# Kernel tuning notes

Measured on AMD Instinct MI355X. Metric: run time of the kernel, lower is better.

## Reference

```python
import jax, jax.numpy as jnp
import numpy as np

K = 8  # knn_graph(k=8, loop=True): self-loop kept, so self is among the k nearest


def knn_idx(x, k):
    # x: [N, F]. Pairwise squared distances via the expansion trick.
    x2 = jnp.sum(x * x, axis=-1)                      # [N]
    d = x2[:, None] + x2[None, :] - 2.0 * (x @ x.T)   # [N, N]
    _, idx = jax.lax.top_k(-d, k)                     # [N, k] nearest (incl. self)
    return idx


def edge_conv(x, idx, W1, b1, W2, b2):
    # PyG EdgeConv: message = nn(cat([x_i, x_j - x_i])), aggr='max'.
    # Every node has exactly k incoming edges, so scatter-max == max over the k axis.
    n, f = x.shape
    k = idx.shape[1]
    xi = x[:, None, :]                                # [N, 1, F] center
    xj = x[idx]                                       # [N, k, F] neighbors (gather)
    e = jnp.concatenate([jnp.broadcast_to(xi, (n, k, f)), xj - xi], axis=-1)  # [N,k,2F]
    h = jax.nn.relu(e @ W1 + b1) @ W2 + b2            # [N, k, out]
    return jnp.max(h, axis=1)                         # [N, out]


def setup_inputs() -> dict:
    key = jax.random.key(0)
    ks = jax.random.split(key, 9)
    B, N, F = 2, 4096, 3
    H0, H1, OUT = 64, 128, 256

    def lin(kw, fan_in, fan_out):
        bound = 1.0 / np.sqrt(fan_in)
        kw1, kw2 = jax.random.split(kw)
        W = jax.random.uniform(kw1, (fan_in, fan_out), jnp.float32, -bound, bound)
        b = jax.random.uniform(kw2, (fan_out,), jnp.float32, -bound, bound)
        return W, b

    W1, b1 = lin(ks[0], 2 * F, H0)
    W2, b2 = lin(ks[1], H0, H1)
    W3, b3 = lin(ks[2], 2 * H1, H1)
    W4, b4 = lin(ks[3], H1, OUT)
    point_cloud = jax.random.normal(ks[4], (B, N, F), jnp.float32)
    return {"point_cloud": point_cloud, "W1": W1, "b1": b1, "W2": W2, "b2": b2,
            "W3": W3, "b3": b3, "W4": W4, "b4": b4}


def reference(point_cloud, W1, b1, W2, b2, W3, b3, W4, b4):
    B, N, F = point_cloud.shape
    pts = point_cloud.reshape(B * N, F)               # knn over ALL B*N points (no batch vec)
    idx = knn_idx(jax.lax.stop_gradient(pts), K)      # [B*N, K]
    x = jax.nn.relu(edge_conv(pts, idx, W1, b1, W2, b2))
    x = edge_conv(x, idx, W3, b3, W4, b4)
    return x.reshape(B, N, -1)
```

## Files before the change

### kernel.cpp

```cpp
#include <hip/hip_runtime.h>

#define NPTS 8192
#define NSLICE 64
#define SLICE_LEN (NPTS / NSLICE)
#define KNN 8
#define SURV_CAP 48
#define TQ 32

typedef short bf16x8 __attribute__((ext_vector_type(8)));
typedef float f32x4 __attribute__((ext_vector_type(4)));

__device__ __forceinline__ unsigned short f2bf(float x) {
  unsigned int u = __float_as_uint(x);
  return (unsigned short)((u + 0x7FFF + ((u >> 16) & 1)) >> 16);
}
__device__ __forceinline__ float bf2f(unsigned short s) {
  return __uint_as_float(((unsigned int)s) << 16);
}

__device__ __forceinline__ float dist_exact(float qx, float qy, float qz,
                                            float q2, float px, float py,
                                            float pz, float p2) {
#pragma clang fp contract(off)
  float dot = __fmaf_rn(qz, pz, __fmaf_rn(qy, py, __fmul_rn(qx, px)));
  float t1 = __fadd_rn(q2, p2);
  return __fadd_rn(t1, __fmul_rn(-2.0f, dot));
}

__device__ __forceinline__ float norm2_exact(float x, float y, float z) {
#pragma clang fp contract(off)
  return __fadd_rn(__fadd_rn(__fmul_rn(x, x), __fmul_rn(y, y)),
                   __fmul_rn(z, z));
}

__device__ __forceinline__ float med3(float a, float b, float c) {
  return __builtin_amdgcn_fmed3f(a, b, c);
}

__device__ __forceinline__ double pack_key(float d, int idx) {
  unsigned int ub = __float_as_uint(d);
  ub ^= (((unsigned int)((int)ub >> 31)) | 0x80000000u);
  unsigned int lo = (ub << 13) | (unsigned int)idx;
  unsigned int hi = 0x3ff00000u | (ub >> 19);
  return __hiloint2double((int)hi, (int)lo);
}

#define KEY_DECL                                                            \
  const double KINF = __longlong_as_double(0x7ff0000000000000LL);           \
  double k0 = KINF, k1 = KINF, k2 = KINF, k3 = KINF, k4 = KINF, k5 = KINF,  \
         k6 = KINF, k7 = KINF;
#define KB1(s)                                                              \
  {                                                                         \
    double mn = fmin(carry, k##s);                                          \
    carry = fmax(carry, k##s);                                              \
    k##s = mn;                                                              \
  }
#define KEY_INSERT(key)                                                     \
  {                                                                         \
    double carry = (key);                                                   \
    KB1(0) KB1(1) KB1(2) KB1(3) KB1(4) KB1(5) KB1(6) KB1(7)                 \
  }

#define VINS(dv)                                                            \
  {                                                                         \
    float dd = (dv);                                                        \
    v7 = med3(dd, v6, v7);                                                  \
    v6 = med3(dd, v5, v6);                                                  \
    v5 = med3(dd, v4, v5);                                                  \
    v4 = med3(dd, v3, v4);                                                  \
    v3 = med3(dd, v2, v3);                                                  \
    v2 = med3(dd, v1, v2);                                                  \
    v1 = med3(dd, v0, v1);                                                  \
    v0 = fminf(dd, v0);                                                     \
  }

#define VDECL                                                               \
  const float FINF = __uint_as_float(0x7f800000u);                          \
  float v0 = FINF, v1 = FINF, v2 = FINF, v3 = FINF, v4 = FINF, v5 = FINF,   \
        v6 = FINF, v7 = FINF;

#define VINS2(dv)                                                           \
  {                                                                         \
    float dd = (dv);                                                        \
    s1 = med3(dd, s0, s1);                                                  \
    s0 = fminf(dd, s0);                                                     \
  }

__global__ __launch_bounds__(256) void prep_kernel(
    const float* __restrict__ W4, const float* __restrict__ pts,
    const float* __restrict__ W2, const float* __restrict__ W3,
    unsigned short* __restrict__ W4ht, unsigned short* __restrict__ W4lt,
    unsigned short* __restrict__ W2th, unsigned short* __restrict__ W2tl,
    unsigned short* __restrict__ W3th, unsigned short* __restrict__ W3tl,
    float4* __restrict__ pts4) {
  const int id = blockIdx.x * 256 + threadIdx.x;
  const int k = id >> 8, c = id & 255;
  {
    float v = W4[k * 256 + c];
    unsigned short hi = f2bf(v);
    unsigned short lo = f2bf(v - bf2f(hi));
    W4ht[c * 128 + k] = hi;
    W4lt[c * 128 + k] = lo;
  }
  {
    float v3 = (c < 128) ? W3[k * 128 + c] : W3[(128 + k) * 128 + (c - 128)];
    unsigned short h3 = f2bf(v3);
    W3th[c * 128 + k] = h3;
    W3tl[c * 128 + k] = f2bf(v3 - bf2f(h3));
  }
  if (id < NPTS) {
    float x = pts[id * 3 + 0];
    float y = pts[id * 3 + 1];
    float z = pts[id * 3 + 2];
    pts4[id] = make_float4(x, y, z, norm2_exact(x, y, z));
    const int kk = id >> 7, cc = id & 127;
    float v2 = W2[kk * 128 + cc];
    unsigned short h2 = f2bf(v2);
    W2th[cc * 64 + kk] = h2;
    W2tl[cc * 64 + kk] = f2bf(v2 - bf2f(h2));
  }
}

__global__ __launch_bounds__(256) void knn_vals_kernel(
    const float4* __restrict__ pts4, float* __restrict__ part_v) {
  __shared__ float4 sp[SLICE_LEN];
  const int t = threadIdx.x;
  const int q = blockIdx.x * 256 + t;
  const int jbase = blockIdx.y * SLICE_LEN;
  for (int p = t; p < SLICE_LEN; p += 256) sp[p] = pts4[jbase + p];
  __syncthreads();
  const float4 qp = pts4[q];
  const float qx = qp.x, qy = qp.y, qz = qp.z, q2 = qp.w;
  const float FINF = __uint_as_float(0x7f800000u);
  float s0 = FINF, s1 = FINF;
  for (int p = 0; p < SLICE_LEN; p += 8) {
    float4 c0 = sp[p + 0];
    float4 c1 = sp[p + 1];
    float4 c2 = sp[p + 2];
    float4 c3 = sp[p + 3];
    float4 c4 = sp[p + 4];
    float4 c5 = sp[p + 5];
    float4 c6 = sp[p + 6];
    float4 c7 = sp[p + 7];
    float d0 = dist_exact(qx, qy, qz, q2, c0.x, c0.y, c0.z, c0.w);
    float d1 = dist_exact(qx, qy, qz, q2, c1.x, c1.y, c1.z, c1.w);
    float d2 = dist_exact(qx, qy, qz, q2, c2.x, c2.y, c2.z, c2.w);
    float d3 = dist_exact(qx, qy, qz, q2, c3.x, c3.y, c3.z, c3.w);
    float d4 = dist_exact(qx, qy, qz, q2, c4.x, c4.y, c4.z, c4.w);
    float d5 = dist_exact(qx, qy, qz, q2, c5.x, c5.y, c5.z, c5.w);
    float d6 = dist_exact(qx, qy, qz, q2, c6.x, c6.y, c6.z, c6.w);
    float d7 = dist_exact(qx, qy, qz, q2, c7.x, c7.y, c7.z, c7.w);
    VINS2(d0);
    VINS2(d1);
    VINS2(d2);
    VINS2(d3);
    VINS2(d4);
    VINS2(d5);
    VINS2(d6);
    VINS2(d7);
  }
  float* o = &part_v[(size_t)(blockIdx.y * 2) * NPTS + q];
  o[0 * NPTS] = s0;
  o[1 * NPTS] = s1;
}

__global__ __launch_bounds__(256) void knn_thresh_kernel(
    const float* __restrict__ part_v, float* __restrict__ thr,
    unsigned long long* __restrict__ mask) {
  __shared__ float v8s[TQ][8][9];
  __shared__ float smin[TQ][65];
  const int t = threadIdx.x;
  const int lq = t >> 3, c = t & 7;
  const int q = blockIdx.x * TQ + lq;
  {
    VDECL;
#pragma unroll
    for (int s8 = 0; s8 < 8; ++s8) {
      const int s = c * 8 + s8;
      const float* col = &part_v[(size_t)(s * 2) * NPTS + q];
      float a0 = col[0 * (size_t)NPTS];
      float a1 = col[1 * (size_t)NPTS];
      smin[lq][s] = a0;
      VINS(a0);
      VINS(a1);
    }
    v8s[lq][c][0] = v0;
    v8s[lq][c][1] = v1;
    v8s[lq][c][2] = v2;
    v8s[lq][c][3] = v3;
    v8s[lq][c][4] = v4;
    v8s[lq][c][5] = v5;
    v8s[lq][c][6] = v6;
    v8s[lq][c][7] = v7;
  }
  __syncthreads();
  if (c == 0) {
    VDECL;
#pragma unroll
    for (int s = 0; s < 8; ++s) {
      VINS(v8s[lq][s][0]);
      VINS(v8s[lq][s][1]);
      VINS(v8s[lq][s][2]);
      VINS(v8s[lq][s][3]);
      VINS(v8s[lq][s][4]);
      VINS(v8s[lq][s][5]);
      VINS(v8s[lq][s][6]);
      VINS(v8s[lq][s][7]);
    }
    const float tcol = v7 + fabsf(v7) * 4e-5f + 1e-20f;
    const float tmask = v7 + fabsf(v7) * 8e-5f + 2e-20f;
    unsigned long long mk = 0;
#pragma unroll
    for (int s = 0; s < NSLICE; ++s) {
      if (smin[lq][s] <= tmask) mk |= (1ull << s);
    }
    thr[q] = tcol;
    mask[q] = mk;
  }
}

__global__ __launch_bounds__(256) void knn_collect_kernel(
    const float4* __restrict__ pts4, const float* __restrict__ thr,
    const unsigned long long* __restrict__ mask, int* __restrict__ nbr) {
  __shared__ double keybuf[4][SURV_CAP];
  __shared__ int scnt[4];
  const int t = threadIdx.x;
  const int wv = t >> 6;
  const int lane = t & 63;
  const int q = blockIdx.x * 4 + wv;
  if (lane == 0) scnt[wv] = 0;
  __syncthreads();
  const float4 qp = pts4[q];
  const float qx = qp.x, qy = qp.y, qz = qp.z, q2 = qp.w;
  const float thrq = thr[q];
  unsigned long long m = mask[q];
  while (m) {
    const int s = (int)__ffsll(m) - 1;
    m &= m - 1;
    const int base = s * SLICE_LEN;
#pragma unroll
    for (int r = 0; r < SLICE_LEN / 64; ++r) {
      const int j = base + r * 64 + lane;
      const float4 cp = pts4[j];
      const float d = dist_exact(qx, qy, qz, q2, cp.x, cp.y, cp.z, cp.w);
      if (d <= thrq) {
        int slot = atomicAdd(&scnt[wv], 1);
        if (slot < SURV_CAP) keybuf[wv][slot] = pack_key(d, j);
      }
    }
  }
  __syncthreads();
  if (lane == 0) {
    int c = scnt[wv];
    if (c > SURV_CAP) c = SURV_CAP;
    KEY_DECL;
    for (int u = 0; u < c; ++u) {
      KEY_INSERT(keybuf[wv][u]);
    }
    int* o = &nbr[q * KNN];
    o[0] = __double2loint(k0) & 0x1fff;
    o[1] = __double2loint(k1) & 0x1fff;
    o[2] = __double2loint(k2) & 0x1fff;
    o[3] = __double2loint(k3) & 0x1fff;
    o[4] = __double2loint(k4) & 0x1fff;
    o[5] = __double2loint(k5) & 0x1fff;
    o[6] = __double2loint(k6) & 0x1fff;
    o[7] = __double2loint(k7) & 0x1fff;
  }
}

__global__ __launch_bounds__(256) void gemm1_fused_kernel(
    const float* __restrict__ pts, const int* __restrict__ nbr,
    const float* __restrict__ W1, const float* __restrict__ b1,
    const unsigned short* __restrict__ W2th,
    const unsigned short* __restrict__ W2tl, const float* __restrict__ b2,
    float* __restrict__ y) {
  __shared__ float es[64][6];
  __shared__ float W1s[6][64];
  __shared__ float b1s[64];
  __shared__ unsigned short H1h[64 * 72];
  __shared__ unsigned short H1l[64 * 72];
  __shared__ unsigned short Wth[64 * 72];
  __shared__ unsigned short Wtl[64 * 72];
  const int t = threadIdx.x;
  const int rowBase = blockIdx.y * 64;
  const int colBase = blockIdx.x * 64;

  for (int idx = t; idx < 384; idx += 256) W1s[idx >> 6][idx & 63] = W1[idx];
  if (t < 64) b1s[t] = b1[t];
  {
    const int colloc = t >> 2, kq = (t & 3) * 16;
    const size_t src = (size_t)(colBase + colloc) * 64 + kq;
    *(uint4*)&Wth[colloc * 72 + kq] = *(const uint4*)&W2th[src];
    *(uint4*)&Wth[colloc * 72 + kq + 8] = *(const uint4*)&W2th[src + 8];
    *(uint4*)&Wtl[colloc * 72 + kq] = *(const uint4*)&W2tl[src];
    *(uint4*)&Wtl[colloc * 72 + kq + 8] = *(const uint4*)&W2tl[src + 8];
  }
  if (t < 64) {
    int e = rowBase + t;
    int i = e >> 3;
    int j = nbr[e];
    float xi0 = pts[i * 3], xi1 = pts[i * 3 + 1], xi2 = pts[i * 3 + 2];
    es[t][0] = xi0;
    es[t][1] = xi1;
    es[t][2] = xi2;
    es[t][3] = pts[j * 3] - xi0;
    es[t][4] = pts[j * 3 + 1] - xi1;
    es[t][5] = pts[j * 3 + 2] - xi2;
  }
  __syncthreads();

  {
    const int e = t & 63, k0 = (t >> 6) * 16;
    const float f0 = es[e][0], f1 = es[e][1], f2 = es[e][2];
    const float f3 = es[e][3], f4 = es[e][4], f5 = es[e][5];
    float h[16];
#pragma unroll
    for (int k = 0; k < 16; ++k) {
      int c = k0 + k;
      float v = b1s[c];
      v = fmaf(f0, W1s[0][c], v);
      v = fmaf(f1, W1s[1][c], v);
      v = fmaf(f2, W1s[2][c], v);
      v = fmaf(f3, W1s[3][c], v);
      v = fmaf(f4, W1s[4][c], v);
      v = fmaf(f5, W1s[5][c], v);
      h[k] = fmaxf(v, 0.0f);
    }
    unsigned int hp[8], lp[8];
#pragma unroll
    for (int u = 0; u < 8; ++u) {
      unsigned short h0 = f2bf(h[2 * u]), h1 = f2bf(h[2 * u + 1]);
      hp[u] = (unsigned int)h0 | ((unsigned int)h1 << 16);
      unsigned short l0 = f2bf(h[2 * u] - bf2f(h0));
      unsigned short l1 = f2bf(h[2 * u + 1] - bf2f(h1));
      lp[u] = (unsigned int)l0 | ((unsigned int)l1 << 16);
    }
    *(uint4*)&H1h[e * 72 + k0] = make_uint4(hp[0], hp[1], hp[2], hp[3]);
    *(uint4*)&H1h[e * 72 + k0 + 8] = make_uint4(hp[4], hp[5], hp[6], hp[7]);
    *(uint4*)&H1l[e * 72 + k0] = make_uint4(lp[0], lp[1], lp[2], lp[3]);
    *(uint4*)&H1l[e * 72 + k0 + 8] = make_uint4(lp[4], lp[5], lp[6], lp[7]);
  }
  __syncthreads();

  const int lane = t & 63, w = t >> 6;
  const int qq = lane >> 4, nidx = lane & 15;
  f32x4 acc[4];
#pragma unroll
  for (int nt = 0; nt < 4; ++nt) acc[nt] = (f32x4){0.f, 0.f, 0.f, 0.f};
  bf16x8 ah0, ah1, al0, al1;
  {
    const int row = w * 16 + nidx;
    ah0 = *(const bf16x8*)&H1h[row * 72 + qq * 8];
    ah1 = *(const bf16x8*)&H1h[row * 72 + 32 + qq * 8];
    al0 = *(const bf16x8*)&H1l[row * 72 + qq * 8];
    al1 = *(const bf16x8*)&H1l[row * 72 + 32 + qq * 8];
  }
#pragma unroll
  for (int nt = 0; nt < 4; ++nt) {
    const int col = nt * 16 + nidx;
    bf16x8 bh0 = *(const bf16x8*)&Wth[col * 72 + qq * 8];
    bf16x8 bh1 = *(const bf16x8*)&Wth[col * 72 + 32 + qq * 8];
    bf16x8 bl0 = *(const bf16x8*)&Wtl[col * 72 + qq * 8];
    bf16x8 bl1 = *(const bf16x8*)&Wtl[col * 72 + 32 + qq * 8];
    acc[nt] = __builtin_amdgcn_mfma_f32_16x16x32_bf16(ah0, bh0, acc[nt], 0, 0, 0);
    acc[nt] = __builtin_amdgcn_mfma_f32_16x16x32_bf16(ah1, bh1, acc[nt], 0, 0, 0);
    acc[nt] = __builtin_amdgcn_mfma_f32_16x16x32_bf16(ah0, bl0, acc[nt], 0, 0, 0);
    acc[nt] = __builtin_amdgcn_mfma_f32_16x16x32_bf16(ah1, bl1, acc[nt], 0, 0, 0);
    acc[nt] = __builtin_amdgcn_mfma_f32_16x16x32_bf16(al0, bh0, acc[nt], 0, 0, 0);
    acc[nt] = __builtin_amdgcn_mfma_f32_16x16x32_bf16(al1, bh1, acc[nt], 0, 0, 0);
  }

  const int pt = blockIdx.y * 8 + 2 * w + (qq >> 1);
#pragma unroll
  for (int nt = 0; nt < 4; ++nt) {
    f32x4 a = acc[nt];
    float m = fmaxf(fmaxf(a[0], a[1]), fmaxf(a[2], a[3]));
    float o = fmaxf(m, __shfl_xor(m, 16, 64));
    if ((qq & 1) == 0) {
      int cg = colBase + nt * 16 + nidx;
      y[(size_t)pt * 128 + cg] = fmaxf(o + b2[cg], 0.0f);
    }
  }
}

__global__ __launch_bounds__(256) void gemm_ac_mfma_kernel(
    const float* __restrict__ y, const unsigned short* __restrict__ W3th,
    const unsigned short* __restrict__ W3tl, const float* __restrict__ bias,
    float* __restrict__ AC) {
  __shared__ unsigned short Ah[128 * 40];
  __shared__ unsigned short Al[128 * 40];
  __shared__ unsigned short Bh[128 * 40];
  __shared__ unsigned short Bl[128 * 40];
  const int t = threadIdx.x;
  const int rowBase = blockIdx.y * 128;
  const int colBase = blockIdx.x * 128;
  const int eloc = t >> 1, hh = t & 1;
  const int kb = hh * 16;
  const int lane = t & 63, w = t >> 6;
  const int q = lane >> 4, nidx = lane & 15;

  f32x4 acc[2][8];
#pragma unroll
  for (int mt = 0; mt < 2; ++mt)
#pragma unroll
    for (int nt = 0; nt < 8; ++nt) acc[mt][nt] = (f32x4){0.f, 0.f, 0.f, 0.f};

  for (int p = 0; p < 4; ++p) {
    const int k0 = p * 32;
    {
      const float* src = &y[(size_t)(rowBase + eloc) * 128 + k0 + kb];
      float h[16];
      *(float4*)&h[0] = *(const float4*)&src[0];
      *(float4*)&h[4] = *(const float4*)&src[4];
      *(float4*)&h[8] = *(const float4*)&src[8];
      *(float4*)&h[12] = *(const float4*)&src[12];
      unsigned int hp[8], lp[8];
#pragma unroll
      for (int u = 0; u < 8; ++u) {
        unsigned short h0 = f2bf(h[2 * u]), h1 = f2bf(h[2 * u + 1]);
        hp[u] = (unsigned int)h0 | ((unsigned int)h1 << 16);
        unsigned short l0 = f2bf(h[2 * u] - bf2f(h0));
        unsigned short l1 = f2bf(h[2 * u + 1] - bf2f(h1));
        lp[u] = (unsigned int)l0 | ((unsigned int)l1 << 16);
      }
      *(uint4*)&Ah[eloc * 40 + kb] = make_uint4(hp[0], hp[1], hp[2], hp[3]);
      *(uint4*)&Ah[eloc * 40 + kb + 8] = make_uint4(hp[4], hp[5], hp[6], hp[7]);
      *(uint4*)&Al[eloc * 40 + kb] = make_uint4(lp[0], lp[1], lp[2], lp[3]);
      *(uint4*)&Al[eloc * 40 + kb + 8] = make_uint4(lp[4], lp[5], lp[6], lp[7]);
    }
    {
      const size_t src = (size_t)(colBase + eloc) * 128 + k0 + kb;
      *(uint4*)&Bh[eloc * 40 + kb] = *(const uint4*)&W3th[src];
      *(uint4*)&Bh[eloc * 40 + kb + 8] = *(const uint4*)&W3th[src + 8];
      *(uint4*)&Bl[eloc * 40 + kb] = *(const uint4*)&W3tl[src];
      *(uint4*)&Bl[eloc * 40 + kb + 8] = *(const uint4*)&W3tl[src + 8];
    }
    __syncthreads();
    bf16x8 ah[2], al[2];
#pragma unroll
    for (int mt = 0; mt < 2; ++mt) {
      int row = w * 32 + mt * 16 + nidx;
      ah[mt] = *(const bf16x8*)&Ah[row * 40 + q * 8];
      al[mt] = *(const bf16x8*)&Al[row * 40 + q * 8];
    }
#pragma unroll
    for (int nt = 0; nt < 8; ++nt) {
      int col = nt * 16 + nidx;
      bf16x8 bh = *(const bf16x8*)&Bh[col * 40 + q * 8];
      bf16x8 bl = *(const bf16x8*)&Bl[col * 40 + q * 8];
#pragma unroll
      for (int mt = 0; mt < 2; ++mt) {
        acc[mt][nt] = __builtin_amdgcn_mfma_f32_16x16x32_bf16(
            ah[mt], bh, acc[mt][nt], 0, 0, 0);
        acc[mt][nt] = __builtin_amdgcn_mfma_f32_16x16x32_bf16(
            ah[mt], bl, acc[mt][nt], 0, 0, 0);
        acc[mt][nt] = __builtin_amdgcn_mfma_f32_16x16x32_bf16(
            al[mt], bh, acc[mt][nt], 0, 0, 0);
      }
    }
    __syncthreads();
  }

#pragma unroll
  for (int mt = 0; mt < 2; ++mt) {
    const int rowb = rowBase + w * 32 + mt * 16 + q * 4;
#pragma unroll
    for (int nt = 0; nt < 8; ++nt) {
      f32x4 a = acc[mt][nt];
      const int cg = colBase + nt * 16 + nidx;
      const float bb = (cg < 128) ? bias[cg] : 0.0f;
#pragma unroll
      for (int reg = 0; reg < 4; ++reg) {
        AC[(size_t)(rowb + reg) * 256 + cg] = a[reg] + bb;
      }
    }
  }
}

__global__ __launch_bounds__(256) void gemm2_mfma_kernel(
    const float* __restrict__ AC, const int* __restrict__ nbr,
    const unsigned short* __restrict__ W4ht,
    const unsigned short* __restrict__ W4lt, const float* __restrict__ b4,
    float* __restrict__ out) {
  __shared__ unsigned short H2h[128 * 40];
  __shared__ unsigned short H2l[128 * 40];
  __shared__ unsigned short Wth[128 * 40];
  __shared__ unsigned short Wtl[128 * 40];
  const int t = threadIdx.x;
  const int rowBase = blockIdx.y * 128;
  const int colBase = blockIdx.x * 128;
  const int eloc = t >> 1, hh = t & 1;
  const int kb = hh * 16;
  const int edge = rowBase + eloc;
  const int ip = edge >> 3;
  const int jp = nbr[edge];
  const float* ai_p = AC + (size_t)ip * 256;
  const float* ci_p = ai_p + 128;
  const float* cj_p = AC + (size_t)jp * 256 + 128;
  const int lane = t & 63;
  const int w = t >> 6;
  const int q = lane >> 4;
  const int nidx = lane & 15;

  f32x4 acc[2][8];
#pragma unroll
  for (int mt = 0; mt < 2; ++mt)
#pragma unroll
    for (int nt = 0; nt < 8; ++nt) acc[mt][nt] = (f32x4){0.f, 0.f, 0.f, 0.f};

  for (int p = 0; p < 4; ++p) {
    const int k0 = p * 32;
    {
      float h2[16];
      const float4* a4 = (const float4*)(ai_p + k0 + kb);
      const float4* c4 = (const float4*)(ci_p + k0 + kb);
      const float4* d4 = (const float4*)(cj_p + k0 + kb);
#pragma unroll
      for (int u = 0; u < 4; ++u) {
        float4 a = a4[u], c = c4[u], d = d4[u];
        h2[u * 4 + 0] = fmaxf(a.x + d.x - c.x, 0.f);
        h2[u * 4 + 1] = fmaxf(a.y + d.y - c.y, 0.f);
        h2[u * 4 + 2] = fmaxf(a.z + d.z - c.z, 0.f);
        h2[u * 4 + 3] = fmaxf(a.w + d.w - c.w, 0.f);
      }
      unsigned int hp[8], lp[8];
#pragma unroll
      for (int u = 0; u < 8; ++u) {
        unsigned short h0 = f2bf(h2[2 * u]), h1 = f2bf(h2[2 * u + 1]);
        hp[u] = (unsigned int)h0 | ((unsigned int)h1 << 16);
        unsigned short l0 = f2bf(h2[2 * u] - bf2f(h0));
        unsigned short l1 = f2bf(h2[2 * u + 1] - bf2f(h1));
        lp[u] = (unsigned int)l0 | ((unsigned int)l1 << 16);
      }
      *(uint4*)&H2h[eloc * 40 + kb] = make_uint4(hp[0], hp[1], hp[2], hp[3]);
      *(uint4*)&H2h[eloc * 40 + kb + 8] =
          make_uint4(hp[4], hp[5], hp[6], hp[7]);
      *(uint4*)&H2l[eloc * 40 + kb] = make_uint4(lp[0], lp[1], lp[2], lp[3]);
      *(uint4*)&H2l[eloc * 40 + kb + 8] =
          make_uint4(lp[4], lp[5], lp[6], lp[7]);
    }
    {
      const size_t src = (size_t)(colBase + eloc) * 128 + k0 + kb;
      *(uint4*)&Wth[eloc * 40 + kb] = *(const uint4*)&W4ht[src];
      *(uint4*)&Wth[eloc * 40 + kb + 8] = *(const uint4*)&W4ht[src + 8];
      *(uint4*)&Wtl[eloc * 40 + kb] = *(const uint4*)&W4lt[src];
      *(uint4*)&Wtl[eloc * 40 + kb + 8] = *(const uint4*)&W4lt[src + 8];
    }
    __syncthreads();
    bf16x8 ah[2], al[2];
#pragma unroll
    for (int mt = 0; mt < 2; ++mt) {
      int row = w * 32 + mt * 16 + nidx;
      ah[mt] = *(const bf16x8*)&H2h[row * 40 + q * 8];
      al[mt] = *(const bf16x8*)&H2l[row * 40 + q * 8];
    }
#pragma unroll
    for (int nt = 0; nt < 8; ++nt) {
      int col = nt * 16 + nidx;
      bf16x8 bh = *(const bf16x8*)&Wth[col * 40 + q * 8];
      bf16x8 bl = *(const bf16x8*)&Wtl[col * 40 + q * 8];
#pragma unroll
      for (int mt = 0; mt < 2; ++mt) {
        acc[mt][nt] = __builtin_amdgcn_mfma_f32_16x16x32_bf16(
            ah[mt], bh, acc[mt][nt], 0, 0, 0);
        acc[mt][nt] = __builtin_amdgcn_mfma_f32_16x16x32_bf16(
            ah[mt], bl, acc[mt][nt], 0, 0, 0);
        acc[mt][nt] = __builtin_amdgcn_mfma_f32_16x16x32_bf16(
            al[mt], bh, acc[mt][nt], 0, 0, 0);
      }
    }
    __syncthreads();
  }

#pragma unroll
  for (int mt = 0; mt < 2; ++mt) {
    const int ebase = rowBase + w * 32 + mt * 16;
    const int pt0 = ebase >> 3;
#pragma unroll
    for (int nt = 0; nt < 8; ++nt) {
      f32x4 a = acc[mt][nt];
      float m = fmaxf(fmaxf(a[0], a[1]), fmaxf(a[2], a[3]));
      float o = fmaxf(m, __shfl_xor(m, 16, 64));
      int cg = colBase + nt * 16 + nidx;
      if (q == 0) {
        out[(size_t)pt0 * 256 + cg] = o + b4[cg];
      } else if (q == 2) {
        out[(size_t)(pt0 + 1) * 256 + cg] = o + b4[cg];
      }
    }
  }
}

extern "C" void kernel_launch(void* const* d_in, const int* in_sizes, int n_in,
                              void* d_out, int out_size, void* d_ws,
                              size_t ws_size, hipStream_t stream) {
  const float* pts = (const float*)d_in[0];
  const float* W1 = (const float*)d_in[1];
  const float* b1 = (const float*)d_in[2];
  const float* W2 = (const float*)d_in[3];
  const float* b2 = (const float*)d_in[4];
  const float* W3 = (const float*)d_in[5];
  const float* b3 = (const float*)d_in[6];
  const float* W4 = (const float*)d_in[7];
  const float* b4 = (const float*)d_in[8];
  float* out = (float*)d_out;

  float* w = (float*)d_ws;
  float* part_v = w;
  float* thr = w + 4194304;
  int* nbr = (int*)(w + 4202496);
  float* y = w + 4268032;
  unsigned long long* mask = (unsigned long long*)(w + 5316608);
  unsigned short* W4ht = (unsigned short*)(w + 5332992);
  unsigned short* W4lt = (unsigned short*)(w + 5349376);
  float4* pts4 = (float4*)(w + 5365760);
  unsigned short* W2th = (unsigned short*)(w + 5398528);
  unsigned short* W2tl = (unsigned short*)(w + 5402624);
  unsigned short* W3th = (unsigned short*)(w + 5406720);
  unsigned short* W3tl = (unsigned short*)(w + 5423104);
  float* AC = w;

  prep_kernel<<<128, 256, 0, stream>>>(W4, pts, W2, W3, W4ht, W4lt, W2th,
                                       W2tl, W3th, W3tl, pts4);

  knn_vals_kernel<<<dim3(32, NSLICE), 256, 0, stream>>>(pts4, part_v);
  knn_thresh_kernel<<<NPTS / TQ, 256, 0, stream>>>(part_v, thr, mask);
  knn_collect_kernel<<<2048, 256, 0, stream>>>(pts4, thr, mask, nbr);

  gemm1_fused_kernel<<<dim3(2, 1024), 256, 0, stream>>>(pts, nbr, W1, b1,
                                                        W2th, W2tl, b2, y);

  gemm_ac_mfma_kernel<<<dim3(2, 64), 256, 0, stream>>>(y, W3th, W3tl, b3, AC);
  gemm2_mfma_kernel<<<dim3(2, 512), 256, 0, stream>>>(AC, nbr, W4ht, W4lt, b4,
                                                      out);
}
```

Before: 156.4 us.

## Fold prep kernel into knn kernels and widen GEMM tiles to full columns

Removes the separate prep launch. The float4 point packing now happens inside knn_vals, and the bf16 hi/lo weight splitting happens in the first 128 blocks of knn_collect. gemm1 and gemm2 now compute all output columns per block instead of splitting columns across two blocks, which avoids re-gathering neighbor rows and recomputing the first MLP layer twice. The costs are more accumulator registers and larger LDS weight tiles, which may reduce occupancy, plus a halved grid size.

```diff
diff --git a/kernel.cpp b/kernel.cpp
--- a/kernel.cpp
+++ b/kernel.cpp
@@ -86,51 +86,24 @@
     s0 = fminf(dd, s0);                                                     \
   }
 
-__global__ __launch_bounds__(256) void prep_kernel(
-    const float* __restrict__ W4, const float* __restrict__ pts,
-    const float* __restrict__ W2, const float* __restrict__ W3,
-    unsigned short* __restrict__ W4ht, unsigned short* __restrict__ W4lt,
-    unsigned short* __restrict__ W2th, unsigned short* __restrict__ W2tl,
-    unsigned short* __restrict__ W3th, unsigned short* __restrict__ W3tl,
+__global__ __launch_bounds__(256) void knn_vals_kernel(
+    const float* __restrict__ pts, float* __restrict__ part_v,
     float4* __restrict__ pts4) {
-  const int id = blockIdx.x * 256 + threadIdx.x;
-  const int k = id >> 8, c = id & 255;
-  {
-    float v = W4[k * 256 + c];
-    unsigned short hi = f2bf(v);
-    unsigned short lo = f2bf(v - bf2f(hi));
-    W4ht[c * 128 + k] = hi;
-    W4lt[c * 128 + k] = lo;
-  }
-  {
-    float v3 = (c < 128) ? W3[k * 128 + c] : W3[(128 + k) * 128 + (c - 128)];
-    unsigned short h3 = f2bf(v3);
-    W3th[c * 128 + k] = h3;
-    W3tl[c * 128 + k] = f2bf(v3 - bf2f(h3));
-  }
-  if (id < NPTS) {
-    float x = pts[id * 3 + 0];
-    float y = pts[id * 3 + 1];
-    float z = pts[id * 3 + 2];
-    pts4[id] = make_float4(x, y, z, norm2_exact(x, y, z));
-    const int kk = id >> 7, cc = id & 127;
-    float v2 = W2[kk * 128 + cc];
-    unsigned short h2 = f2bf(v2);
-    W2th[cc * 64 + kk] = h2;
-    W2tl[cc * 64 + kk] = f2bf(v2 - bf2f(h2));
-  }
-}
-
-__global__ __launch_bounds__(256) void knn_vals_kernel(
-    const float4* __restrict__ pts4, float* __restrict__ part_v) {
   __shared__ float4 sp[SLICE_LEN];
   const int t = threadIdx.x;
   const int q = blockIdx.x * 256 + t;
   const int jbase = blockIdx.y * SLICE_LEN;
-  for (int p = t; p < SLICE_LEN; p += 256) sp[p] = pts4[jbase + p];
+  for (int p = t; p < SLICE_LEN; p += 256) {
+    float x = pts[(jbase + p) * 3 + 0];
+    float yy = pts[(jbase + p) * 3 + 1];
+    float z = pts[(jbase + p) * 3 + 2];
+    float4 v = make_float4(x, yy, z, norm2_exact(x, yy, z));
+    sp[p] = v;
+    if (blockIdx.x == 0) pts4[jbase + p] = v;
+  }
   __syncthreads();
-  const float4 qp = pts4[q];
-  const float qx = qp.x, qy = qp.y, qz = qp.z, q2 = qp.w;
+  const float qx = pts[q * 3 + 0], qy = pts[q * 3 + 1], qz = pts[q * 3 + 2];
+  const float q2 = norm2_exact(qx, qy, qz);
   const float FINF = __uint_as_float(0x7f800000u);
   float s0 = FINF, s1 = FINF;
   for (int p = 0; p < SLICE_LEN; p += 8) {
@@ -221,10 +194,38 @@
 
 __global__ __launch_bounds__(256) void knn_collect_kernel(
     const float4* __restrict__ pts4, const float* __restrict__ thr,
-    const unsigned long long* __restrict__ mask, int* __restrict__ nbr) {
+    const unsigned long long* __restrict__ mask, int* __restrict__ nbr,
+    const float* __restrict__ W2, const float* __restrict__ W3,
+    const float* __restrict__ W4, unsigned short* __restrict__ W2th,
+    unsigned short* __restrict__ W2tl, unsigned short* __restrict__ W3th,
+    unsigned short* __restrict__ W3tl, unsigned short* __restrict__ W4ht,
+    unsigned short* __restrict__ W4lt) {
   __shared__ double keybuf[4][SURV_CAP];
   __shared__ int scnt[4];
   const int t = threadIdx.x;
+  if (blockIdx.x < 128) {
+    const int id = blockIdx.x * 256 + t;
+    const int k = id >> 8, c = id & 255;
+    {
+      float v = W4[k * 256 + c];
+      unsigned short hi = f2bf(v);
+      W4ht[c * 128 + k] = hi;
+      W4lt[c * 128 + k] = f2bf(v - bf2f(hi));
+    }
+    {
+      float v3 = (c < 128) ? W3[k * 128 + c] : W3[(128 + k) * 128 + (c - 128)];
+      unsigned short h3 = f2bf(v3);
+      W3th[c * 128 + k] = h3;
+      W3tl[c * 128 + k] = f2bf(v3 - bf2f(h3));
+    }
+    if (id < NPTS) {
+      const int kk = id >> 7, cc = id & 127;
+      float v2 = W2[kk * 128 + cc];
+      unsigned short h2 = f2bf(v2);
+      W2th[cc * 64 + kk] = h2;
+      W2tl[cc * 64 + kk] = f2bf(v2 - bf2f(h2));
+    }
+  }
   const int wv = t >> 6;
   const int lane = t & 63;
   const int q = blockIdx.x * 4 + wv;
@@ -280,21 +281,24 @@
   __shared__ float b1s[64];
   __shared__ unsigned short H1h[64 * 72];
   __shared__ unsigned short H1l[64 * 72];
-  __shared__ unsigned short Wth[64 * 72];
-  __shared__ unsigned short Wtl[64 * 72];
+  __shared__ unsigned short Wth[128 * 72];
+  __shared__ unsigned short Wtl[128 * 72];
   const int t = threadIdx.x;
-  const int rowBase = blockIdx.y * 64;
-  const int colBase = blockIdx.x * 64;
+  const int rowBase = blockIdx.x * 64;
 
   for (int idx = t; idx < 384; idx += 256) W1s[idx >> 6][idx & 63] = W1[idx];
   if (t < 64) b1s[t] = b1[t];
   {
-    const int colloc = t >> 2, kq = (t & 3) * 16;
-    const size_t src = (size_t)(colBase + colloc) * 64 + kq;
+    const int colloc = t >> 1, kq = (t & 1) * 32;
+    const size_t src = (size_t)colloc * 64 + kq;
     *(uint4*)&Wth[colloc * 72 + kq] = *(const uint4*)&W2th[src];
     *(uint4*)&Wth[colloc * 72 + kq + 8] = *(const uint4*)&W2th[src + 8];
+    *(uint4*)&Wth[colloc * 72 + kq + 16] = *(const uint4*)&W2th[src + 16];
+    *(uint4*)&Wth[colloc * 72 + kq + 24] = *(const uint4*)&W2th[src + 24];
     *(uint4*)&Wtl[colloc * 72 + kq] = *(const uint4*)&W2tl[src];
     *(uint4*)&Wtl[colloc * 72 + kq + 8] = *(const uint4*)&W2tl[src + 8];
+    *(uint4*)&Wtl[colloc * 72 + kq + 16] = *(const uint4*)&W2tl[src + 16];
+    *(uint4*)&Wtl[colloc * 72 + kq + 24] = *(const uint4*)&W2tl[src + 24];
   }
   if (t < 64) {
     int e = rowBase + t;
@@ -345,9 +349,9 @@
 
   const int lane = t & 63, w = t >> 6;
   const int qq = lane >> 4, nidx = lane & 15;
-  f32x4 acc[4];
-#pragma unroll
-  for (int nt = 0; nt < 4; ++nt) acc[nt] = (f32x4){0.f, 0.f, 0.f, 0.f};
+  f32x4 acc[8];
+#pragma unroll
+  for (int nt = 0; nt < 8; ++nt) acc[nt] = (f32x4){0.f, 0.f, 0.f, 0.f};
   bf16x8 ah0, ah1, al0, al1;
   {
     const int row = w * 16 + nidx;
@@ -357,7 +361,7 @@
     al1 = *(const bf16x8*)&H1l[row * 72 + 32 + qq * 8];
   }
 #pragma unroll
-  for (int nt = 0; nt < 4; ++nt) {
+  for (int nt = 0; nt < 8; ++nt) {
     const int col = nt * 16 + nidx;
     bf16x8 bh0 = *(const bf16x8*)&Wth[col * 72 + qq * 8];
     bf16x8 bh1 = *(const bf16x8*)&Wth[col * 72 + 32 + qq * 8];
@@ -371,14 +375,14 @@
     acc[nt] = __builtin_amdgcn_mfma_f32_16x16x32_bf16(al1, bh1, acc[nt], 0, 0, 0);
   }
 
-  const int pt = blockIdx.y * 8 + 2 * w + (qq >> 1);
-#pragma unroll
-  for (int nt = 0; nt < 4; ++nt) {
+  const int pt = blockIdx.x * 8 + 2 * w + (qq >> 1);
+#pragma unroll
+  for (int nt = 0; nt < 8; ++nt) {
     f32x4 a = acc[nt];
     float m = fmaxf(fmaxf(a[0], a[1]), fmaxf(a[2], a[3]));
     float o = fmaxf(m, __shfl_xor(m, 16, 64));
     if ((qq & 1) == 0) {
-      int cg = colBase + nt * 16 + nidx;
+      int cg = nt * 16 + nidx;
       y[(size_t)pt * 128 + cg] = fmaxf(o + b2[cg], 0.0f);
     }
   }
@@ -485,11 +489,10 @@
     float* __restrict__ out) {
   __shared__ unsigned short H2h[128 * 40];
   __shared__ unsigned short H2l[128 * 40];
-  __shared__ unsigned short Wth[128 * 40];
-  __shared__ unsigned short Wtl[128 * 40];
+  __shared__ unsigned short Wth[256 * 40];
+  __shared__ unsigned short Wtl[256 * 40];
   const int t = threadIdx.x;
-  const int rowBase = blockIdx.y * 128;
-  const int colBase = blockIdx.x * 128;
+  const int rowBase = blockIdx.x * 128;
   const int eloc = t >> 1, hh = t & 1;
   const int kb = hh * 16;
   const int edge = rowBase + eloc;
@@ -503,11 +506,11 @@
   const int q = lane >> 4;
   const int nidx = lane & 15;
 
-  f32x4 acc[2][8];
+  f32x4 acc[2][16];
 #pragma unroll
   for (int mt = 0; mt < 2; ++mt)
 #pragma unroll
-    for (int nt = 0; nt < 8; ++nt) acc[mt][nt] = (f32x4){0.f, 0.f, 0.f, 0.f};
+    for (int nt = 0; nt < 16; ++nt) acc[mt][nt] = (f32x4){0.f, 0.f, 0.f, 0.f};
 
   for (int p = 0; p < 4; ++p) {
     const int k0 = p * 32;
@@ -541,11 +544,15 @@
           make_uint4(lp[4], lp[5], lp[6], lp[7]);
     }
     {
-      const size_t src = (size_t)(colBase + eloc) * 128 + k0 + kb;
-      *(uint4*)&Wth[eloc * 40 + kb] = *(const uint4*)&W4ht[src];
-      *(uint4*)&Wth[eloc * 40 + kb + 8] = *(const uint4*)&W4ht[src + 8];
-      *(uint4*)&Wtl[eloc * 40 + kb] = *(const uint4*)&W4lt[src];
-      *(uint4*)&Wtl[eloc * 40 + kb + 8] = *(const uint4*)&W4lt[src + 8];
+      const size_t src = (size_t)t * 128 + k0;
+      *(uint4*)&Wth[t * 40 + 0] = *(const uint4*)&W4ht[src + 0];
+      *(uint4*)&Wth[t * 40 + 8] = *(const uint4*)&W4ht[src + 8];
+      *(uint4*)&Wth[t * 40 + 16] = *(const uint4*)&W4ht[src + 16];
+      *(uint4*)&Wth[t * 40 + 24] = *(const uint4*)&W4ht[src + 24];
+      *(uint4*)&Wtl[t * 40 + 0] = *(const uint4*)&W4lt[src + 0];
+      *(uint4*)&Wtl[t * 40 + 8] = *(const uint4*)&W4lt[src + 8];
+      *(uint4*)&Wtl[t * 40 + 16] = *(const uint4*)&W4lt[src + 16];
+      *(uint4*)&Wtl[t * 40 + 24] = *(const uint4*)&W4lt[src + 24];
     }
     __syncthreads();
     bf16x8 ah[2], al[2];
@@ -556,7 +563,7 @@
       al[mt] = *(const bf16x8*)&H2l[row * 40 + q * 8];
     }
 #pragma unroll
-    for (int nt = 0; nt < 8; ++nt) {
+    for (int nt = 0; nt < 16; ++nt) {
       int col = nt * 16 + nidx;
       bf16x8 bh = *(const bf16x8*)&Wth[col * 40 + q * 8];
       bf16x8 bl = *(const bf16x8*)&Wtl[col * 40 + q * 8];
@@ -578,11 +585,11 @@
     const int ebase = rowBase + w * 32 + mt * 16;
     const int pt0 = ebase >> 3;
 #pragma unroll
-    for (int nt = 0; nt < 8; ++nt) {
+    for (int nt = 0; nt < 16; ++nt) {
       f32x4 a = acc[mt][nt];
       float m = fmaxf(fmaxf(a[0], a[1]), fmaxf(a[2], a[3]));
       float o = fmaxf(m, __shfl_xor(m, 16, 64));
-      int cg = colBase + nt * 16 + nidx;
+      int cg = nt * 16 + nidx;
       if (q == 0) {
         out[(size_t)pt0 * 256 + cg] = o + b4[cg];
       } else if (q == 2) {
@@ -621,17 +628,15 @@
   unsigned short* W3tl = (unsigned short*)(w + 5423104);
   float* AC = w;
 
-  prep_kernel<<<128, 256, 0, stream>>>(W4, pts, W2, W3, W4ht, W4lt, W2th,
-                                       W2tl, W3th, W3tl, pts4);
-
-  knn_vals_kernel<<<dim3(32, NSLICE), 256, 0, stream>>>(pts4, part_v);
+  knn_vals_kernel<<<dim3(32, NSLICE), 256, 0, stream>>>(pts, part_v, pts4);
   knn_thresh_kernel<<<NPTS / TQ, 256, 0, stream>>>(part_v, thr, mask);
-  knn_collect_kernel<<<2048, 256, 0, stream>>>(pts4, thr, mask, nbr);
-
-  gemm1_fused_kernel<<<dim3(2, 1024), 256, 0, stream>>>(pts, nbr, W1, b1,
-                                                        W2th, W2tl, b2, y);
+  knn_collect_kernel<<<2048, 256, 0, stream>>>(pts4, thr, mask, nbr, W2, W3,
+                                               W4, W2th, W2tl, W3th, W3tl,
+                                               W4ht, W4lt);
+
+  gemm1_fused_kernel<<<1024, 256, 0, stream>>>(pts, nbr, W1, b1, W2th, W2tl,
+                                               b2, y);
 
   gemm_ac_mfma_kernel<<<dim3(2, 64), 256, 0, stream>>>(y, W3th, W3tl, b3, AC);
-  gemm2_mfma_kernel<<<dim3(2, 512), 256, 0, stream>>>(AC, nbr, W4ht, W4lt, b4,
-                                                      out);
-}
+  gemm2_mfma_kernel<<<512, 256, 0, stream>>>(AC, nbr, W4ht, W4lt, b4, out);
+}
```

Result: slower. 170.6 us (+9.1%).
